# Kernel optimization log

Hardware: AMD Instinct MI355X
Metric: run time of the kernel (lower is better)

## Reference

```python
import jax, jax.numpy as jnp
import numpy as np

N_NODES = 100000
MAX_DEG = 64
NODE_DIM = 256
V = 8192
NUM_SAMPLES = 16


def setup_inputs() -> dict:
    key = jax.random.key(0)
    k1, k2, k3, k4 = jax.random.split(key, 4)
    ids = jax.random.randint(k1, (V,), 0, N_NODES, dtype=jnp.int32)
    adj_info = jax.random.randint(k2, (N_NODES, MAX_DEG), 0, N_NODES, dtype=jnp.int32)
    features = jax.random.normal(k3, (N_NODES, NODE_DIM), dtype=jnp.float32)
    W = jax.random.normal(k4, (NODE_DIM, NODE_DIM), dtype=jnp.float32) * 0.05
    b = jnp.zeros((NODE_DIM,), dtype=jnp.float32)
    return {"ids": ids, "adj_info": adj_info, "features": features, "W": W, "b": b,
            "num_samples": NUM_SAMPLES}


def reference(ids, adj_info, features, W, b, num_samples):
    n_nodes, neig_num = adj_info.shape
    group_dim = neig_num // num_samples
    K = group_dim * num_samples  # tf.slice to a multiple of num_samples
    v = ids.shape[0]

    adj_lists = adj_info[ids][:, :K]                     # [V, K] neighbor ids
    v_f = features[ids]                                  # [V, d]
    n_f = features[adj_lists]                            # [V, K, d]

    # linear sampler branch: dense(v_f) then matmul with neighbor feats, relu
    l = v_f @ W + b                                      # [V, d]
    scores = jax.nn.relu(jnp.einsum('vd,vkd->vk', l, n_f))  # [V, K]

    # grouped argmin: pick one neighbor per group of group_dim
    scores = scores.reshape(v, num_samples, group_dim)   # [V, S, G]
    idx_y = jnp.argmin(scores, axis=-1).astype(jnp.int32)  # [V, S]
    idx_y = idx_y + (jnp.arange(num_samples, dtype=jnp.int32) * group_dim)[None, :]

    sel = jnp.take_along_axis(adj_lists, idx_y, axis=1)  # [V, S]

    # count non-padding neighbors (padding sentinel = n_nodes - 1)
    nonpad = jnp.where(sel == n_nodes - 1,
                       jnp.zeros(sel.shape, jnp.float32),
                       jnp.ones(sel.shape, jnp.float32))
    numnz = nonpad.sum(axis=1)                           # [V]
    att = jnp.ones(sel.shape, jnp.float32)
    return sel, att, numnz, numnz
```

## Files before the change

### kernel.cpp

```cpp
#include <hip/hip_runtime.h>
#include <hip/hip_bf16.h>

#define N_NODES   100000
#define MAX_DEG   64
#define NODE_DIM  256
#define NUM_V     8192
#define NSAMP     16
#define GROUP_DIM 4
#define SENTINEL  (N_NODES - 1)

#define BM 64
#define BN 64
#define BK 16

__global__ __launch_bounds__(256) void gemm_l_kernel(
    const int* __restrict__ ids,
    const float* __restrict__ features,
    const float* __restrict__ W,
    const float* __restrict__ bias,
    float* __restrict__ l_out) {
  __shared__ float As[BK][BM];
  __shared__ float Ws[BK][BN];
  __shared__ int   nid_s[BM];

  const int tid  = threadIdx.x;
  const int row0 = blockIdx.x * BM;
  const int col0 = blockIdx.y * BN;

  if (tid < BM) nid_s[tid] = ids[row0 + tid];
  __syncthreads();

  const int tx = tid & 15;
  const int ty = tid >> 4;

  const int am = tid >> 2;
  const int ak = (tid & 3) * 4;
  const int wk = tid >> 4;
  const int wn = (tid & 15) * 4;

  const size_t a_base = (size_t)nid_s[am] * NODE_DIM + ak;

  float acc[4][4] = {};

  for (int k0 = 0; k0 < NODE_DIM; k0 += BK) {
    const float4 av = *reinterpret_cast<const float4*>(&features[a_base + k0]);
    As[ak + 0][am] = av.x;
    As[ak + 1][am] = av.y;
    As[ak + 2][am] = av.z;
    As[ak + 3][am] = av.w;
    const float4 wv = *reinterpret_cast<const float4*>(
        &W[(size_t)(k0 + wk) * NODE_DIM + col0 + wn]);
    *reinterpret_cast<float4*>(&Ws[wk][wn]) = wv;
    __syncthreads();

#pragma unroll
    for (int k = 0; k < BK; ++k) {
      float ra[4], rb[4];
#pragma unroll
      for (int i = 0; i < 4; ++i) ra[i] = As[k][ty * 4 + i];
#pragma unroll
      for (int j = 0; j < 4; ++j) rb[j] = Ws[k][tx * 4 + j];
#pragma unroll
      for (int i = 0; i < 4; ++i)
#pragma unroll
        for (int j = 0; j < 4; ++j) acc[i][j] += ra[i] * rb[j];
    }
    __syncthreads();
  }

#pragma unroll
  for (int i = 0; i < 4; ++i) {
    const int m = row0 + ty * 4 + i;
#pragma unroll
    for (int j = 0; j < 4; ++j) {
      const int n = col0 + tx * 4 + j;
      l_out[(size_t)m * NODE_DIM + n] = acc[i][j] + bias[n];
    }
  }
}

__global__ __launch_bounds__(256) void sampler_kernel(
    const int* __restrict__ ids,
    const int* __restrict__ adj,
    const float* __restrict__ features,
    const float* __restrict__ l,
    float* __restrict__ out_sel,
    float* __restrict__ out_att,
    float* __restrict__ out_nz1,
    float* __restrict__ out_nz2) {
  __shared__ int   adj_s[MAX_DEG];
  __shared__ float scores_s[MAX_DEG];
  __shared__ float nonpad_s[NSAMP];

  const int v   = blockIdx.x;
  const int tid = threadIdx.x;
  const int nid = ids[v];

  if (tid < MAX_DEG) adj_s[tid] = adj[(size_t)nid * MAX_DEG + tid];
  __syncthreads();

  const int wave = tid >> 6;
  const int lane = tid & 63;

  const float4 lv =
      *reinterpret_cast<const float4*>(&l[(size_t)v * NODE_DIM + lane * 4]);

  for (int kk = 0; kk < 16; ++kk) {
    const int k  = wave * 16 + kk;
    const int nb = adj_s[k];
    const float4 f = *reinterpret_cast<const float4*>(
        &features[(size_t)nb * NODE_DIM + lane * 4]);
    float p = lv.x * f.x + lv.y * f.y + lv.z * f.z + lv.w * f.w;
#pragma unroll
    for (int off = 32; off > 0; off >>= 1) p += __shfl_xor(p, off, 64);
    if (lane == 0) scores_s[k] = p > 0.0f ? p : 0.0f;
  }
  __syncthreads();

  if (tid < NSAMP) {
    const int s = tid;
    float best = scores_s[s * GROUP_DIM];
    int   bi   = 0;
#pragma unroll
    for (int g = 1; g < GROUP_DIM; ++g) {
      const float sc = scores_s[s * GROUP_DIM + g];
      if (sc < best) { best = sc; bi = g; }
    }
    const int selid = adj_s[s * GROUP_DIM + bi];
    out_sel[(size_t)v * NSAMP + s] = (float)selid;
    out_att[(size_t)v * NSAMP + s] = 1.0f;
    nonpad_s[s] = (selid == SENTINEL) ? 0.0f : 1.0f;
  }
  __syncthreads();

  if (tid == 0) {
    float nz = 0.0f;
#pragma unroll
    for (int s = 0; s < NSAMP; ++s) nz += nonpad_s[s];
    out_nz1[v] = nz;
    out_nz2[v] = nz;
  }
}

extern "C" void kernel_launch(void* const* d_in, const int* in_sizes, int n_in,
                              void* d_out, int out_size, void* d_ws,
                              size_t ws_size, hipStream_t stream) {
  const int*   ids      = (const int*)d_in[0];
  const int*   adj      = (const int*)d_in[1];
  const float* features = (const float*)d_in[2];
  const float* W        = (const float*)d_in[3];
  const float* bias     = (const float*)d_in[4];

  float* l_ws = (float*)d_ws;

  float* out     = (float*)d_out;
  float* out_sel = out;
  float* out_att = out + (size_t)NUM_V * NSAMP;
  float* out_nz1 = out + (size_t)2 * NUM_V * NSAMP;
  float* out_nz2 = out_nz1 + NUM_V;

  gemm_l_kernel<<<dim3(NUM_V / BM, NODE_DIM / BN), 256, 0, stream>>>(
      ids, features, W, bias, l_ws);
  sampler_kernel<<<NUM_V, 256, 0, stream>>>(ids, adj, features, l_ws, out_sel,
                                            out_att, out_nz1, out_nz2);
}
```

Measured before the change: 240.5 us.

## Restructure sampler to 4-lane-per-neighbor dot products with shuffle argmin

The sampler kernel now gives each neighbor 4 lanes that each cover 64 elements of the dot product, instead of looping over neighbors one at a time with full-wave reductions. This puts all 64 neighbor row loads in flight at once and cuts the shuffle reduction to two steps. The grouped argmin is done with lane shuffles instead of a shared-memory pass, and the l vector is staged in shared memory. The GEMM kernel also switches to float4 shared-memory reads and float4 bias-added stores. Each lane now reads a 16-byte chunk with a 64-byte stride within a row, which may coalesce less well than contiguous per-wave row reads.

Measured after the change: 239.9 us. About the same (-0.3%).

```diff
diff --git a/kernel.cpp b/kernel.cpp
--- a/kernel.cpp
+++ b/kernel.cpp
@@ -48,34 +48,35 @@
     As[ak + 1][am] = av.y;
     As[ak + 2][am] = av.z;
     As[ak + 3][am] = av.w;
-    const float4 wv = *reinterpret_cast<const float4*>(
+    *reinterpret_cast<float4*>(&Ws[wk][wn]) = *reinterpret_cast<const float4*>(
         &W[(size_t)(k0 + wk) * NODE_DIM + col0 + wn]);
-    *reinterpret_cast<float4*>(&Ws[wk][wn]) = wv;
     __syncthreads();
 
 #pragma unroll
     for (int k = 0; k < BK; ++k) {
-      float ra[4], rb[4];
-#pragma unroll
-      for (int i = 0; i < 4; ++i) ra[i] = As[k][ty * 4 + i];
-#pragma unroll
-      for (int j = 0; j < 4; ++j) rb[j] = Ws[k][tx * 4 + j];
+      const float4 ra = *reinterpret_cast<const float4*>(&As[k][ty * 4]);
+      const float4 rb = *reinterpret_cast<const float4*>(&Ws[k][tx * 4]);
+      const float a[4] = {ra.x, ra.y, ra.z, ra.w};
+      const float b[4] = {rb.x, rb.y, rb.z, rb.w};
 #pragma unroll
       for (int i = 0; i < 4; ++i)
 #pragma unroll
-        for (int j = 0; j < 4; ++j) acc[i][j] += ra[i] * rb[j];
+        for (int j = 0; j < 4; ++j) acc[i][j] += a[i] * b[j];
     }
     __syncthreads();
   }
 
+  const float4 bv =
+      *reinterpret_cast<const float4*>(&bias[col0 + tx * 4]);
 #pragma unroll
   for (int i = 0; i < 4; ++i) {
     const int m = row0 + ty * 4 + i;
-#pragma unroll
-    for (int j = 0; j < 4; ++j) {
-      const int n = col0 + tx * 4 + j;
-      l_out[(size_t)m * NODE_DIM + n] = acc[i][j] + bias[n];
-    }
+    float4 o;
+    o.x = acc[i][0] + bv.x;
+    o.y = acc[i][1] + bv.y;
+    o.z = acc[i][2] + bv.z;
+    o.w = acc[i][3] + bv.w;
+    *reinterpret_cast<float4*>(&l_out[(size_t)m * NODE_DIM + col0 + tx * 4]) = o;
   }
 }
 
@@ -88,55 +89,63 @@
     float* __restrict__ out_att,
     float* __restrict__ out_nz1,
     float* __restrict__ out_nz2) {
+  __shared__ float l_s[NODE_DIM];
   __shared__ int   adj_s[MAX_DEG];
-  __shared__ float scores_s[MAX_DEG];
-  __shared__ float nonpad_s[NSAMP];
+  __shared__ float nz_s[NSAMP];
 
   const int v   = blockIdx.x;
   const int tid = threadIdx.x;
   const int nid = ids[v];
 
+  l_s[tid] = l[(size_t)v * NODE_DIM + tid];
   if (tid < MAX_DEG) adj_s[tid] = adj[(size_t)nid * MAX_DEG + tid];
   __syncthreads();
 
   const int wave = tid >> 6;
   const int lane = tid & 63;
+  const int q    = lane >> 2;
+  const int sub  = lane & 3;
+  const int k    = wave * 16 + q;
 
-  const float4 lv =
-      *reinterpret_cast<const float4*>(&l[(size_t)v * NODE_DIM + lane * 4]);
+  const int nb = adj_s[k];
+  const float* __restrict__ rowp = features + (size_t)nb * NODE_DIM + sub * 4;
+  const float* __restrict__ lp   = l_s + sub * 4;
 
-  for (int kk = 0; kk < 16; ++kk) {
-    const int k  = wave * 16 + kk;
-    const int nb = adj_s[k];
-    const float4 f = *reinterpret_cast<const float4*>(
-        &features[(size_t)nb * NODE_DIM + lane * 4]);
-    float p = lv.x * f.x + lv.y * f.y + lv.z * f.z + lv.w * f.w;
+  float p = 0.0f;
 #pragma unroll
-    for (int off = 32; off > 0; off >>= 1) p += __shfl_xor(p, off, 64);
-    if (lane == 0) scores_s[k] = p > 0.0f ? p : 0.0f;
+  for (int c = 0; c < 16; ++c) {
+    const float4 f  = *reinterpret_cast<const float4*>(rowp + c * 16);
+    const float4 lv = *reinterpret_cast<const float4*>(lp + c * 16);
+    p += f.x * lv.x + f.y * lv.y + f.z * lv.z + f.w * lv.w;
   }
-  __syncthreads();
+  p += __shfl_xor(p, 1, 64);
+  p += __shfl_xor(p, 2, 64);
+  float s = p > 0.0f ? p : 0.0f;
 
-  if (tid < NSAMP) {
-    const int s = tid;
-    float best = scores_s[s * GROUP_DIM];
-    int   bi   = 0;
-#pragma unroll
-    for (int g = 1; g < GROUP_DIM; ++g) {
-      const float sc = scores_s[s * GROUP_DIM + g];
-      if (sc < best) { best = sc; bi = g; }
-    }
-    const int selid = adj_s[s * GROUP_DIM + bi];
-    out_sel[(size_t)v * NSAMP + s] = (float)selid;
-    out_att[(size_t)v * NSAMP + s] = 1.0f;
-    nonpad_s[s] = (selid == SENTINEL) ? 0.0f : 1.0f;
+  int g = q & 3;
+  {
+    float os = __shfl_xor(s, 4, 64);
+    int   og = __shfl_xor(g, 4, 64);
+    if (os < s || (os == s && og < g)) { s = os; g = og; }
+    os = __shfl_xor(s, 8, 64);
+    og = __shfl_xor(g, 8, 64);
+    if (os < s || (os == s && og < g)) { s = os; g = og; }
+  }
+
+  if ((lane & 15) == 0) {
+    const int gl    = lane >> 4;
+    const int s_idx = wave * 4 + gl;
+    const int selid = adj_s[s_idx * GROUP_DIM + g];
+    out_sel[(size_t)v * NSAMP + s_idx] = (float)selid;
+    out_att[(size_t)v * NSAMP + s_idx] = 1.0f;
+    nz_s[s_idx] = (selid == SENTINEL) ? 0.0f : 1.0f;
   }
   __syncthreads();
 
   if (tid == 0) {
     float nz = 0.0f;
 #pragma unroll
-    for (int s = 0; s < NSAMP; ++s) nz += nonpad_s[s];
+    for (int t = 0; t < NSAMP; ++t) nz += nz_s[t];
     out_nz1[v] = nz;
     out_nz2[v] = nz;
   }
```
